# Kernel tuning notes

Measured on AMD Instinct MI355X. Metric: run time of the kernel, lower is better.

## Reference

```python
import jax, jax.numpy as jnp
import numpy as np

D_MODEL, D_FF, H, DK, DV = 1024, 4096, 16, 64, 64
B, S = 16, 512
EPS = 1e-6

def layer_norm(x, g, b):
    mu = jnp.mean(x, axis=-1, keepdims=True)
    var = jnp.var(x, axis=-1, keepdims=True)
    return (x - mu) / jnp.sqrt(var + EPS) * g + b

def setup_inputs() -> dict:
    key = jax.random.key(0)
    ks = jax.random.split(key, 16)
    def lin(k, fan_in, fan_out):
        lim = 1.0 / np.sqrt(fan_in)
        kw, kb = jax.random.split(k)
        W = jax.random.uniform(kw, (fan_in, fan_out), jnp.float32, -lim, lim)
        b = jax.random.uniform(kb, (fan_out,), jnp.float32, -lim, lim)
        return W, b
    Wq, bq = lin(ks[0], D_MODEL, DK * H)
    Wk, bk = lin(ks[1], D_MODEL, DK * H)
    Wv, bv = lin(ks[2], D_MODEL, DV * H)
    Wo, bo = lin(ks[3], DV * H, D_MODEL)
    w1, b1 = lin(ks[4], D_MODEL, D_FF)   # conv1d k=1 == pointwise linear
    w2, b2 = lin(ks[5], D_FF, D_MODEL)
    return {
        "enc_inputs": jax.random.normal(ks[6], (B, S, D_MODEL), jnp.float32),
        "Wq": Wq, "bq": bq, "Wk": Wk, "bk": bk, "Wv": Wv, "bv": bv,
        "Wo": Wo, "bo": bo,
        "ln1_g": jnp.ones((D_MODEL,), jnp.float32), "ln1_b": jnp.zeros((D_MODEL,), jnp.float32),
        "w1": w1, "b1": b1, "w2": w2, "b2": b2,
        "ln2_g": jnp.ones((D_MODEL,), jnp.float32), "ln2_b": jnp.zeros((D_MODEL,), jnp.float32),
        "mask": jax.random.randint(ks[7], (B, S), 0, 2, jnp.int32),
        "max_neighbors": S,
    }

def reference(enc_inputs, Wq, bq, Wk, bk, Wv, bv, Wo, bo, ln1_g, ln1_b,
              w1, b1, w2, b2, ln2_g, ln2_b, mask, max_neighbors):
    x = enc_inputs  # [B, S, D]
    residual = x
    # projections -> [B, H, S, d]
    q = (x @ Wq + bq).reshape(B, S, H, DK).transpose(0, 2, 1, 3)
    k = (x @ Wk + bk).reshape(B, S, H, DK).transpose(0, 2, 1, 3)
    v = (x @ Wv + bv).reshape(B, S, H, DV).transpose(0, 2, 1, 3)
    scores = jnp.einsum('bhqd,bhkd->bhqk', q, k) / np.sqrt(DK)
    pad = (mask == 0)[:, None, None, :]  # [B,1,1,S] broadcasts over heads & query
    scores = jnp.where(pad, jnp.float32(-1e9), scores)
    attn = jax.nn.softmax(scores, axis=-1)
    ctx = jnp.einsum('bhqk,bhkd->bhqd', attn, v)
    ctx = ctx.transpose(0, 2, 1, 3).reshape(B, S, H * DV)
    ctx = ctx @ Wo + bo
    ctx = layer_norm(ctx + residual, ln1_g, ln1_b)
    # position-wise FFN (conv1d kernel=1 == linear)
    ff = jax.nn.relu(ctx @ w1 + b1) @ w2 + b2
    out = layer_norm(ff + ctx, ln2_g, ln2_b)
    return out, attn
```

## Files before the change

kernel.cpp:

```cpp
#include <hip/hip_runtime.h>
#include <hip/hip_bf16.h>

typedef unsigned short u16;
typedef __bf16 bf16x8 __attribute__((ext_vector_type(8)));
typedef float f32x4 __attribute__((ext_vector_type(4)));

static __device__ __forceinline__ float b2f(u16 x) {
    unsigned int u = ((unsigned int)x) << 16;
    float f; __builtin_memcpy(&f, &u, 4); return f;
}
static __device__ __forceinline__ float b2f_u32(unsigned int u) {
    float f; __builtin_memcpy(&f, &u, 4); return f;
}
static __device__ __forceinline__ u16 f2b(float f) {
    unsigned int u; __builtin_memcpy(&u, &f, 4);
    unsigned int lsb = (u >> 16) & 1u;
    u += 0x7fffu + lsb;
    return (u16)(u >> 16);
}

static __device__ __forceinline__ void gload16(const u16* g, u16* l) {
    __builtin_amdgcn_global_load_lds(
        (const __attribute__((address_space(1))) unsigned int*)g,
        (__attribute__((address_space(3))) unsigned int*)l, 16, 0, 0);
}

__global__ __launch_bounds__(256) void transpose_f2b(const float* __restrict__ src,
                                                     u16* __restrict__ dst,
                                                     int R, int C) {
    __shared__ u16 tile[32][33];
    int c0 = blockIdx.x * 32, r0 = blockIdx.y * 32;
    int tx = threadIdx.x & 31, ty = threadIdx.x >> 5;
    for (int i = ty; i < 32; i += 8) {
        int r = r0 + i, c = c0 + tx;
        tile[i][tx] = (r < R && c < C) ? f2b(src[(long)r * C + c]) : (u16)0;
    }
    __syncthreads();
    for (int i = ty; i < 32; i += 8) {
        int c = c0 + i, r = r0 + tx;
        if (c < C && r < R) dst[(long)c * R + r] = tile[tx][i];
    }
}

__global__ __launch_bounds__(256) void concat3(const float* a, const float* b, const float* c,
                                               float* out) {
    int i = blockIdx.x * 256 + threadIdx.x;
    if (i < 1024) out[i] = a[i];
    else if (i < 2048) out[i] = b[i - 1024];
    else if (i < 3072) out[i] = c[i - 2048];
}

__global__ __launch_bounds__(256) void conv_f2b(const float* __restrict__ src,
                                                u16* __restrict__ dst, long n) {
    long i = ((long)blockIdx.x * 256 + threadIdx.x) * 4;
    if (i >= n) return;
    float4 f = *(const float4*)(src + i);
    ushort4 o;
    o.x = f2b(f.x); o.y = f2b(f.y); o.z = f2b(f.z); o.w = f2b(f.w);
    *(ushort4*)(dst + i) = o;
}

__global__ __launch_bounds__(512, 1) void gemm_bt256(
    const u16* __restrict__ A, const u16* __restrict__ B,
    const float* __restrict__ bias, u16* __restrict__ C,
    int M, int N, int K, int lda, int ldb, int ldc, int relu, int nbx) {
    __shared__ __align__(16) u16 lds[2][4][8192];

    int nwg = gridDim.x;
    int id = blockIdx.x;
    int swz = (id & 7) * (nwg >> 3) + (id >> 3);
    int bx = swz % nbx, by = swz / nbx;
    long m0 = (long)by * 256, n0 = (long)bx * 256;

    int tid = threadIdx.x, lane = tid & 63, wave = tid >> 6;
    int lrow = lane & 15, quad = lane >> 4;
    int wm2 = wave >> 2;
    int wn2 = wave & 3;

    int laneRd = (lrow * 64 + quad * 16) ^ (((lrow >> 3) & 1) << 5);
    int Sl = (lane * 16) ^ (((lane >> 5) & 1) << 5);
    int wr = (Sl >> 6) & 15;
    int wb = Sl & 63;

    f32x4 acc[8][4];
#pragma unroll
    for (int i = 0; i < 8; i++)
#pragma unroll
        for (int j = 0; j < 4; j++) acc[i][j] = (f32x4){0.f, 0.f, 0.f, 0.f};
    bf16x8 af[4][2], bfr[2][2];

#define STAGE_HT(nb, ht, kt) do {                                              \
    const char* _gb = ((ht) < 2)                                               \
        ? (const char*)(A + (m0 + (ht) * 128) * lda)                           \
        : (const char*)(B + (n0 + ((ht) - 2) * 128) * ldb);                    \
    long _ld = (long)(((ht) < 2) ? lda : ldb) * 2;                             \
    _Pragma("unroll")                                                          \
    for (int j = 0; j < 2; j++) {                                              \
        int sub = j * 8 + wave;                                                \
        int srow = (sub >> 1) * 16 + wr;                                       \
        int scolb = (sub & 1) * 64 + wb;                                       \
        gload16((const u16*)(_gb + (long)srow * _ld + (long)(kt) * 128 + scolb),\
                &lds[nb][ht][sub << 9]);                                       \
    }                                                                          \
} while (0)

#define DSLOAD_A(qm) do {                                                      \
    const char* _p = _ab + ((qm) << 14);                                       \
    _Pragma("unroll") for (int mi = 0; mi < 4; mi++)                           \
    _Pragma("unroll") for (int kk = 0; kk < 2; kk++)                           \
        af[mi][kk] = *(const bf16x8*)(_p + ((mi * 4 + kk) << 10));             \
} while (0)

#define DSLOAD_B(qn) do {                                                      \
    const char* _p = _bb + ((qn) << 14);                                       \
    _Pragma("unroll") for (int ni = 0; ni < 2; ni++)                           \
    _Pragma("unroll") for (int kk = 0; kk < 2; kk++)                           \
        bfr[ni][kk] = *(const bf16x8*)(_p + ((ni * 8 + kk) << 10));            \
} while (0)

#define DOMFMA(qm, qn) do {                                                    \
    __builtin_amdgcn_s_setprio(1);                                             \
    _Pragma("unroll") for (int mi = 0; mi < 4; mi++)                           \
    _Pragma("unroll") for (int ni = 0; ni < 2; ni++)                           \
    _Pragma("unroll") for (int kk = 0; kk < 2; kk++)                           \
        acc[(qm) * 4 + mi][(qn) * 2 + ni] =                                    \
            __builtin_amdgcn_mfma_f32_16x16x32_bf16(                           \
                af[mi][kk], bfr[ni][kk], acc[(qm) * 4 + mi][(qn) * 2 + ni],    \
                0, 0, 0);                                                      \
    __builtin_amdgcn_s_setprio(0);                                             \
} while (0)

#define MIDBAR()  do { __builtin_amdgcn_s_barrier(); __builtin_amdgcn_sched_barrier(0); } while (0)
#define ENDBAR()  do { __builtin_amdgcn_sched_barrier(0); __builtin_amdgcn_s_barrier(); } while (0)

    int NT = K >> 6;
    STAGE_HT(0, 0, 0);
    STAGE_HT(0, 2, 0);
    STAGE_HT(0, 1, 0);
    STAGE_HT(0, 3, 0);

    for (int t = 0; t < NT - 1; t++) {
        int cur = t & 1, nxt = cur ^ 1;
        const char* _ab = (const char*)&lds[cur][0][0] + (wm2 << 11) + laneRd;
        const char* _bb = (const char*)&lds[cur][2][0] + (wn2 << 11) + laneRd;
        STAGE_HT(nxt, 0, t + 1);
        asm volatile("s_waitcnt vmcnt(6)" ::: "memory");
        MIDBAR();
        DSLOAD_A(0); DSLOAD_B(0); DOMFMA(0, 0);
        ENDBAR();
        STAGE_HT(nxt, 2, t + 1);
        asm volatile("s_waitcnt vmcnt(6)" ::: "memory");
        MIDBAR();
        DSLOAD_A(1); DOMFMA(1, 0);
        ENDBAR();
        STAGE_HT(nxt, 1, t + 1);
        asm volatile("s_waitcnt vmcnt(6)" ::: "memory");
        MIDBAR();
        DSLOAD_B(1); DOMFMA(1, 1);
        ENDBAR();
        STAGE_HT(nxt, 3, t + 1);
        MIDBAR();
        DSLOAD_A(0); DOMFMA(0, 1);
        ENDBAR();
    }
    {
        int cur = (NT - 1) & 1;
        const char* _ab = (const char*)&lds[cur][0][0] + (wm2 << 11) + laneRd;
        const char* _bb = (const char*)&lds[cur][2][0] + (wn2 << 11) + laneRd;
        asm volatile("s_waitcnt vmcnt(4)" ::: "memory");
        MIDBAR();
        DSLOAD_A(0); DSLOAD_B(0); DOMFMA(0, 0);
        ENDBAR();
        asm volatile("s_waitcnt vmcnt(2)" ::: "memory");
        MIDBAR();
        DSLOAD_A(1); DOMFMA(1, 0);
        ENDBAR();
        asm volatile("s_waitcnt vmcnt(0)" ::: "memory");
        MIDBAR();
        DSLOAD_B(1); DOMFMA(1, 1);
        ENDBAR();
        DSLOAD_A(0); DOMFMA(0, 1);
    }

#pragma unroll
    for (int mg = 0; mg < 8; mg++) {
        long row0 = m0 + (long)(((mg >> 2) * 8 + (mg & 3) * 2 + wm2) * 16 + quad * 4);
#pragma unroll
        for (int ng = 0; ng < 4; ng++) {
            long col = n0 + ((ng >> 1) * 8 + (ng & 1) * 4 + wn2) * 16 + lrow;
            float bv = bias ? bias[col] : 0.f;
#pragma unroll
            for (int r = 0; r < 4; r++) {
                float v = acc[mg][ng][r] + bv;
                if (relu) v = fmaxf(v, 0.f);
                C[(row0 + r) * ldc + col] = f2b(v);
            }
        }
    }
#undef STAGE_HT
#undef DSLOAD_A
#undef DSLOAD_B
#undef DOMFMA
}

__global__ __launch_bounds__(512, 1) void gemm_btn(
    const u16* __restrict__ A, const u16* __restrict__ B,
    const float* __restrict__ bias, u16* __restrict__ C,
    int K, int lda, int ldb, int ldc, int relu, int nbx) {
    __shared__ __align__(16) u16 lds[2][3][8192];

    int nwg = gridDim.x;
    int id = blockIdx.x;
    int swz = (id & 7) * (nwg >> 3) + (id >> 3);
    int bx = swz % nbx, by = swz / nbx;
    long m0 = (long)by * 128, n0 = (long)bx * 256;

    int tid = threadIdx.x, lane = tid & 63, wave = tid >> 6;
    int lrow = lane & 15, quad = lane >> 4;
    int wm2 = wave >> 2;
    int wn2 = wave & 3;

    int laneRd = (lrow * 64 + quad * 16) ^ (((lrow >> 3) & 1) << 5);
    int Sl = (lane * 16) ^ (((lane >> 5) & 1) << 5);
    int wr = (Sl >> 6) & 15;
    int wb = Sl & 63;

    f32x4 acc[4][4];
#pragma unroll
    for (int i = 0; i < 4; i++)
#pragma unroll
        for (int j = 0; j < 4; j++) acc[i][j] = (f32x4){0.f, 0.f, 0.f, 0.f};
    bf16x8 af[4][2], bfr[2][2];

#define STAGE_HT(nb, ht, kt) do {                                              \
    const char* _gb = ((ht) == 0)                                              \
        ? (const char*)(A + m0 * lda)                                          \
        : (const char*)(B + (n0 + ((ht) - 1) * 128) * ldb);                    \
    long _ld = (long)(((ht) == 0) ? lda : ldb) * 2;                            \
    _Pragma("unroll")                                                          \
    for (int j = 0; j < 2; j++) {                                              \
        int sub = j * 8 + wave;                                                \
        int srow = (sub >> 1) * 16 + wr;                                       \
        int scolb = (sub & 1) * 64 + wb;                                       \
        gload16((const u16*)(_gb + (long)srow * _ld + (long)(kt) * 128 + scolb),\
                &lds[nb][ht][sub << 9]);                                       \
    }                                                                          \
} while (0)

#define DSLOAD_A() do {                                                        \
    _Pragma("unroll") for (int mi = 0; mi < 4; mi++)                           \
    _Pragma("unroll") for (int kk = 0; kk < 2; kk++)                           \
        af[mi][kk] = *(const bf16x8*)(_ab + ((mi * 4 + kk) << 10));            \
} while (0)

#define DSLOAD_B(qn) do {                                                      \
    const char* _p = _b0 + (qn) * 16384;                                       \
    _Pragma("unroll") for (int ni = 0; ni < 2; ni++)                           \
    _Pragma("unroll") for (int kk = 0; kk < 2; kk++)                           \
        bfr[ni][kk] = *(const bf16x8*)(_p + ((ni * 8 + kk) << 10));            \
} while (0)

#define DOMFMA(qn) do {                                                        \
    __builtin_amdgcn_s_setprio(1);                                             \
    _Pragma("unroll") for (int mi = 0; mi < 4; mi++)                           \
    _Pragma("unroll") for (int ni = 0; ni < 2; ni++)                           \
    _Pragma("unroll") for (int kk = 0; kk < 2; kk++)                           \
        acc[mi][(qn) * 2 + ni] =                                               \
            __builtin_amdgcn_mfma_f32_16x16x32_bf16(                           \
                af[mi][kk], bfr[ni][kk], acc[mi][(qn) * 2 + ni], 0, 0, 0);     \
    __builtin_amdgcn_s_setprio(0);                                             \
} while (0)

    int NT = K >> 6;
    STAGE_HT(0, 0, 0);
    STAGE_HT(0, 1, 0);
    STAGE_HT(0, 2, 0);

    for (int t = 0; t < NT - 1; t++) {
        int cur = t & 1, nxt = cur ^ 1;
        const char* _ab = (const char*)&lds[cur][0][0] + (wm2 << 11) + laneRd;
        const char* _b0 = (const char*)&lds[cur][1][0] + (wn2 << 11) + laneRd;
        STAGE_HT(nxt, 0, t + 1);
        asm volatile("s_waitcnt vmcnt(4)" ::: "memory");
        MIDBAR();
        DSLOAD_A(); DSLOAD_B(0); DOMFMA(0);
        ENDBAR();
        STAGE_HT(nxt, 1, t + 1);
        STAGE_HT(nxt, 2, t + 1);
        asm volatile("s_waitcnt vmcnt(6)" ::: "memory");
        MIDBAR();
        DSLOAD_B(1); DOMFMA(1);
        ENDBAR();
    }
    {
        int cur = (NT - 1) & 1;
        const char* _ab = (const char*)&lds[cur][0][0] + (wm2 << 11) + laneRd;
        const char* _b0 = (const char*)&lds[cur][1][0] + (wn2 << 11) + laneRd;
        asm volatile("s_waitcnt vmcnt(2)" ::: "memory");
        MIDBAR();
        DSLOAD_A(); DSLOAD_B(0); DOMFMA(0);
        ENDBAR();
        asm volatile("s_waitcnt vmcnt(0)" ::: "memory");
        MIDBAR();
        DSLOAD_B(1); DOMFMA(1);
    }

#pragma unroll
    for (int mi = 0; mi < 4; mi++) {
        long row0 = m0 + (long)((mi * 2 + wm2) * 16 + quad * 4);
#pragma unroll
        for (int ng = 0; ng < 4; ng++) {
            long col = n0 + ((ng >> 1) * 8 + (ng & 1) * 4 + wn2) * 16 + lrow;
            float bv = bias ? bias[col] : 0.f;
#pragma unroll
            for (int r = 0; r < 4; r++) {
                float v = acc[mi][ng][r] + bv;
                if (relu) v = fmaxf(v, 0.f);
                C[(row0 + r) * ldc + col] = f2b(v);
            }
        }
    }
#undef STAGE_HT
#undef DSLOAD_A
#undef DSLOAD_B
#undef DOMFMA
#undef MIDBAR
#undef ENDBAR
}

__global__ __launch_bounds__(256) void split_v(const u16* __restrict__ qkv,
                                               u16* __restrict__ vT) {
    __shared__ u16 tile[32][33];
    int bh = blockIdx.z;
    int b = bh >> 4, h = bh & 15;
    int s0 = blockIdx.x * 32;
    int d0 = blockIdx.y * 32;
    int tx = threadIdx.x & 31, ty = threadIdx.x >> 5;
    for (int i = ty; i < 32; i += 8)
        tile[i][tx] = qkv[((long)(b * 512 + s0 + i)) * 3072 + 2048 + h * 64 + d0 + tx];
    __syncthreads();
    for (int i = ty; i < 32; i += 8)
        vT[((long)bh * 64 + d0 + i) * 512 + s0 + tx] = tile[tx][i];
}

__global__ __launch_bounds__(256) void attn_fused(
    const u16* __restrict__ qkv, const u16* __restrict__ vT,
    const int* __restrict__ mask, float* __restrict__ attnOut,
    u16* __restrict__ ctx) {
    __shared__ __align__(16) u16 s_tile[64][72];
    __shared__ __align__(16) u16 s_p[4][16][136];
    __shared__ unsigned long long m_bits[8];

    int id = blockIdx.x;
    int t_ = id >> 3;
    int mtile = t_ & 7;
    int bh = (id & 7) + ((t_ >> 3) << 3);
    int b = bh >> 4, h = bh & 15;
    int tid = threadIdx.x, lane = tid & 63, wave = tid >> 6;
    int lrow = lane & 15, quad = lane >> 4;
    int m0 = mtile * 64;

    const u16* Qbase = qkv + (long)(b * 512) * 3072 + h * 64;
    const u16* Kbase = Qbase + 1024;

    {
        int i0 = wave * 64 + lane;
        unsigned long long bl0 = __ballot(mask[b * 512 + i0] != 0);
        if (lane == 0) m_bits[wave] = bl0;
        unsigned long long bl1 = __ballot(mask[b * 512 + 256 + i0] != 0);
        if (lane == 0) m_bits[4 + wave] = bl1;
    }

#pragma unroll
    for (int i = 0; i < 2; i++) {
        int idx = i * 256 + tid;
        int r = idx >> 3, c = (idx & 7) * 8;
        *(uint4*)&s_tile[r][c] = *(const uint4*)(Qbase + (long)(m0 + r) * 3072 + c);
    }
    __syncthreads();
    bf16x8 qf[2];
    qf[0] = *(const bf16x8*)&s_tile[wave * 16 + lrow][0 + quad * 8];
    qf[1] = *(const bf16x8*)&s_tile[wave * 16 + lrow][32 + quad * 8];

    f32x4 sacc[32];
#pragma unroll
    for (int t = 0; t < 32; t++) sacc[t] = (f32x4){0.f, 0.f, 0.f, 0.f};

#pragma unroll
    for (int t = 0; t < 32; t++) {
        const u16* krow = Kbase + (long)(t * 16 + lrow) * 3072 + quad * 8;
        bf16x8 b0 = *(const bf16x8*)krow;
        bf16x8 b1 = *(const bf16x8*)(krow + 32);
        sacc[t] = __builtin_amdgcn_mfma_f32_16x16x32_bf16(qf[0], b0, sacc[t], 0, 0, 0);
        sacc[t] = __builtin_amdgcn_mfma_f32_16x16x32_bf16(qf[1], b1, sacc[t], 0, 0, 0);
    }

    float mx[4] = {-3.0e38f, -3.0e38f, -3.0e38f, -3.0e38f};
#pragma unroll
    for (int t = 0; t < 32; t++) {
        int col = t * 16 + lrow;
        int on = (int)((m_bits[col >> 6] >> (col & 63)) & 1ull);
#pragma unroll
        for (int r = 0; r < 4; r++) {
            float s = on ? sacc[t][r] * 0.125f : -1e9f;
            sacc[t][r] = s;
            mx[r] = fmaxf(mx[r], s);
        }
    }
#pragma unroll
    for (int off = 1; off < 16; off <<= 1)
#pragma unroll
        for (int r = 0; r < 4; r++) mx[r] = fmaxf(mx[r], __shfl_xor(mx[r], off));
    float sm[4] = {0.f, 0.f, 0.f, 0.f};
#pragma unroll
    for (int t = 0; t < 32; t++)
#pragma unroll
        for (int r = 0; r < 4; r++) {
            float e = __expf(sacc[t][r] - mx[r]);
            sacc[t][r] = e;
            sm[r] += e;
        }
#pragma unroll
    for (int off = 1; off < 16; off <<= 1)
#pragma unroll
        for (int r = 0; r < 4; r++) sm[r] += __shfl_xor(sm[r], off);
#pragma unroll
    for (int r = 0; r < 4; r++) sm[r] = 1.0f / sm[r];
#pragma unroll
    for (int t = 0; t < 32; t++)
#pragma unroll
        for (int r = 0; r < 4; r++) sacc[t][r] *= sm[r];

    f32x4 cacc[4];
#pragma unroll
    for (int ni = 0; ni < 4; ni++) cacc[ni] = (f32x4){0.f, 0.f, 0.f, 0.f};
    const u16* vh = vT + (long)bh * 64 * 512;
    int prr = lane >> 5;
    int pcc = lane & 31;

    for (int nc = 0; nc < 4; nc++) {
#pragma unroll
        for (int t2 = 0; t2 < 8; t2++) {
            int t = nc * 8 + t2;
#pragma unroll
            for (int r = 0; r < 4; r++)
                s_p[wave][quad * 4 + r][t2 * 16 + lrow] = f2b(sacc[t][r]);
        }

        {
            float* abase = attnOut + (long)bh * 512 * 512
                         + (long)(m0 + wave * 16) * 512 + nc * 128;
#pragma unroll
            for (int i = 0; i < 8; i++) {
                int row = i * 2 + prr;
                uint2 pv = *(const uint2*)&s_p[wave][row][pcc * 4];
                float4 o;
                o.x = b2f_u32(pv.x << 16);
                o.y = b2f_u32(pv.x & 0xffff0000u);
                o.z = b2f_u32(pv.y << 16);
                o.w = b2f_u32(pv.y & 0xffff0000u);
                *(float4*)(abase + (long)row * 512 + pcc * 4) = o;
            }
        }

#pragma unroll
        for (int kk = 0; kk < 4; kk++) {
            bf16x8 pf = *(const bf16x8*)&s_p[wave][lrow][kk * 32 + quad * 8];
#pragma unroll
            for (int ni = 0; ni < 4; ni++) {
                bf16x8 vf = *(const bf16x8*)(vh + (long)(ni * 16 + lrow) * 512 + nc * 128 + kk * 32 + quad * 8);
                cacc[ni] = __builtin_amdgcn_mfma_f32_16x16x32_bf16(pf, vf, cacc[ni], 0, 0, 0);
            }
        }
    }

    u16* crow = ctx + (long)(b * 512 + m0 + wave * 16 + quad * 4) * 1024 + h * 64 + lrow;
#pragma unroll
    for (int ni = 0; ni < 4; ni++)
#pragma unroll
        for (int r = 0; r < 4; r++) crow[(long)r * 1024 + ni * 16] = f2b(cacc[ni][r]);
}

__global__ __launch_bounds__(256) void add_ln(const u16* __restrict__ a,
                                              const void* __restrict__ r, int r_fp32,
                                              const float* __restrict__ g,
                                              const float* __restrict__ beta,
                                              void* __restrict__ out, int out_fp32) {
    long row = blockIdx.x;
    const u16* pa = a + row * 1024;
    int tid = threadIdx.x;
    float v[4];
    float sum = 0.f, sq = 0.f;
#pragma unroll
    for (int j = 0; j < 4; j++) {
        int c = tid + j * 256;
        float rv = r_fp32 ? ((const float*)r)[row * 1024 + c]
                          : b2f(((const u16*)r)[row * 1024 + c]);
        float x = b2f(pa[c]) + rv;
        v[j] = x;
        sum += x;
        sq += x * x;
    }
#pragma unroll
    for (int off = 32; off >= 1; off >>= 1) {
        sum += __shfl_xor(sum, off);
        sq += __shfl_xor(sq, off);
    }
    __shared__ float red[2][4];
    int wave = tid >> 6, lane = tid & 63;
    if (lane == 0) { red[0][wave] = sum; red[1][wave] = sq; }
    __syncthreads();
    sum = red[0][0] + red[0][1] + red[0][2] + red[0][3];
    sq = red[1][0] + red[1][1] + red[1][2] + red[1][3];
    float mu = sum * (1.f / 1024.f);
    float var = sq * (1.f / 1024.f) - mu * mu;
    float rstd = rsqrtf(var + 1e-6f);
#pragma unroll
    for (int j = 0; j < 4; j++) {
        int c = tid + j * 256;
        float y = (v[j] - mu) * rstd * g[c] + beta[c];
        if (out_fp32) ((float*)out)[row * 1024 + c] = y;
        else ((u16*)out)[row * 1024 + c] = f2b(y);
    }
}

extern "C" void kernel_launch(void* const* d_in, const int* in_sizes, int n_in,
                              void* d_out, int out_size, void* d_ws, size_t ws_size,
                              hipStream_t stream) {
    const float* x   = (const float*)d_in[0];
    const float* Wq  = (const float*)d_in[1];
    const float* bq  = (const float*)d_in[2];
    const float* Wk  = (const float*)d_in[3];
    const float* bk  = (const float*)d_in[4];
    const float* Wv  = (const float*)d_in[5];
    const float* bv  = (const float*)d_in[6];
    const float* Wo  = (const float*)d_in[7];
    const float* bo  = (const float*)d_in[8];
    const float* g1  = (const float*)d_in[9];
    const float* be1 = (const float*)d_in[10];
    const float* w1  = (const float*)d_in[11];
    const float* b1  = (const float*)d_in[12];
    const float* w2  = (const float*)d_in[13];
    const float* b2  = (const float*)d_in[14];
    const float* g2  = (const float*)d_in[15];
    const float* be2 = (const float*)d_in[16];
    const int* mask  = (const int*)d_in[17];

    float* out = (float*)d_out;
    float* attn = out + (long)8192 * 1024;

    char* w = (char*)d_ws;
    auto alloc = [&](size_t bytes) {
        char* p = w;
        w += (bytes + 255) & ~(size_t)255;
        return p;
    };
    u16* WqkvT = (u16*)alloc(3072L * 1024 * 2);
    u16* WoT   = (u16*)alloc(1024L * 1024 * 2);
    u16* w1T   = (u16*)alloc(4096L * 1024 * 2);
    u16* w2T   = (u16*)alloc(1024L * 4096 * 2);
    float* bqkv = (float*)alloc(3072L * 4);
    u16* xb    = (u16*)alloc(8192L * 1024 * 2);
    char* P1 = alloc(8192L * 4096 * 2);
    u16* qkv = (u16*)P1;
    u16* ff  = (u16*)P1;
    char* P2 = alloc(256L * 64 * 512 * 2);
    u16* vT = (u16*)P2;
    u16* y2 = (u16*)P2;
    u16* ctx = (u16*)alloc(8192L * 1024 * 2);
    u16* x1  = (u16*)alloc(8192L * 1024 * 2);
    u16* y   = (u16*)alloc(8192L * 1024 * 2);

    dim3 blk(256);

    transpose_f2b<<<dim3(32, 32), blk, 0, stream>>>(Wq, WqkvT, 1024, 1024);
    transpose_f2b<<<dim3(32, 32), blk, 0, stream>>>(Wk, WqkvT + 1024L * 1024, 1024, 1024);
    transpose_f2b<<<dim3(32, 32), blk, 0, stream>>>(Wv, WqkvT + 2048L * 1024, 1024, 1024);
    transpose_f2b<<<dim3(32, 32), blk, 0, stream>>>(Wo, WoT, 1024, 1024);
    transpose_f2b<<<dim3(128, 32), blk, 0, stream>>>(w1, w1T, 1024, 4096);
    transpose_f2b<<<dim3(32, 128), blk, 0, stream>>>(w2, w2T, 4096, 1024);
    concat3<<<12, blk, 0, stream>>>(bq, bk, bv, bqkv);
    conv_f2b<<<8192, blk, 0, stream>>>(x, xb, 8192L * 1024);

    gemm_bt256<<<dim3(384), dim3(512), 0, stream>>>(
        xb, WqkvT, bqkv, qkv, 8192, 3072, 1024, 1024, 1024, 3072, 0, 12);

    split_v<<<dim3(16, 2, 256), blk, 0, stream>>>(qkv, vT);

    attn_fused<<<dim3(2048), blk, 0, stream>>>(qkv, vT, mask, attn, ctx);

    gemm_btn<<<dim3(256), dim3(512), 0, stream>>>(
        ctx, WoT, bo, y, 1024, 1024, 1024, 1024, 0, 4);

    add_ln<<<8192, blk, 0, stream>>>(y, x, 1, g1, be1, x1, 0);

    gemm_bt256<<<dim3(512), dim3(512), 0, stream>>>(
        x1, w1T, b1, ff, 8192, 4096, 1024, 1024, 1024, 4096, 1, 16);

    gemm_btn<<<dim3(256), dim3(512), 0, stream>>>(
        ff, w2T, b2, y2, 4096, 4096, 4096, 1024, 0, 4);

    add_ln<<<8192, blk, 0, stream>>>(y2, x1, 0, g2, be2, out, 1);
}
```

Baseline: 870.0 us.

## Stage K tiles through LDS with register prefetch in attention QK^T

Before this, each wave loaded the K rows it needed straight from global memory, so every one of the 4 waves fetched the whole K block. Now the block loads K cooperatively in 128-row chunks into a larger LDS tile, and the next chunk is prefetched into registers while the MFMAs run on the current one. The goal is to cut redundant global K traffic and hide load latency. In exchange it doubles the s_tile LDS footprint, adds barriers per chunk and holds extra prefetch registers, which could lower occupancy in a kernel that already keeps 32 accumulators live.

After: 829.2 us. 4.7% less time.

```diff
diff --git a/kernel.cpp b/kernel.cpp
--- a/kernel.cpp
+++ b/kernel.cpp
@@ -347,7 +347,7 @@
     const u16* __restrict__ qkv, const u16* __restrict__ vT,
     const int* __restrict__ mask, float* __restrict__ attnOut,
     u16* __restrict__ ctx) {
-    __shared__ __align__(16) u16 s_tile[64][72];
+    __shared__ __align__(16) u16 s_tile[128][72];
     __shared__ __align__(16) u16 s_p[4][16][136];
     __shared__ unsigned long long m_bits[8];
 
@@ -377,22 +377,48 @@
         int r = idx >> 3, c = (idx & 7) * 8;
         *(uint4*)&s_tile[r][c] = *(const uint4*)(Qbase + (long)(m0 + r) * 3072 + c);
     }
+    uint4 kreg[4];
+#pragma unroll
+    for (int i = 0; i < 4; i++) {
+        int idx = i * 256 + tid;
+        int r = idx >> 3, c = (idx & 7) * 8;
+        kreg[i] = *(const uint4*)(Kbase + (long)r * 3072 + c);
+    }
     __syncthreads();
     bf16x8 qf[2];
     qf[0] = *(const bf16x8*)&s_tile[wave * 16 + lrow][0 + quad * 8];
     qf[1] = *(const bf16x8*)&s_tile[wave * 16 + lrow][32 + quad * 8];
+    __syncthreads();
 
     f32x4 sacc[32];
 #pragma unroll
     for (int t = 0; t < 32; t++) sacc[t] = (f32x4){0.f, 0.f, 0.f, 0.f};
 
-#pragma unroll
-    for (int t = 0; t < 32; t++) {
-        const u16* krow = Kbase + (long)(t * 16 + lrow) * 3072 + quad * 8;
-        bf16x8 b0 = *(const bf16x8*)krow;
-        bf16x8 b1 = *(const bf16x8*)(krow + 32);
-        sacc[t] = __builtin_amdgcn_mfma_f32_16x16x32_bf16(qf[0], b0, sacc[t], 0, 0, 0);
-        sacc[t] = __builtin_amdgcn_mfma_f32_16x16x32_bf16(qf[1], b1, sacc[t], 0, 0, 0);
+    for (int nc = 0; nc < 4; nc++) {
+#pragma unroll
+        for (int i = 0; i < 4; i++) {
+            int idx = i * 256 + tid;
+            int r = idx >> 3, c = (idx & 7) * 8;
+            *(uint4*)&s_tile[r][c] = kreg[i];
+        }
+        __syncthreads();
+        if (nc < 3) {
+#pragma unroll
+            for (int i = 0; i < 4; i++) {
+                int idx = i * 256 + tid;
+                int r = idx >> 3, c = (idx & 7) * 8;
+                kreg[i] = *(const uint4*)(Kbase + (long)((nc + 1) * 128 + r) * 3072 + c);
+            }
+        }
+#pragma unroll
+        for (int ni = 0; ni < 8; ni++) {
+            bf16x8 b0 = *(const bf16x8*)&s_tile[ni * 16 + lrow][0 + quad * 8];
+            bf16x8 b1 = *(const bf16x8*)&s_tile[ni * 16 + lrow][32 + quad * 8];
+            int t = nc * 8 + ni;
+            sacc[t] = __builtin_amdgcn_mfma_f32_16x16x32_bf16(qf[0], b0, sacc[t], 0, 0, 0);
+            sacc[t] = __builtin_amdgcn_mfma_f32_16x16x32_bf16(qf[1], b1, sacc[t], 0, 0, 0);
+        }
+        __syncthreads();
     }
 
     float mx[4] = {-3.0e38f, -3.0e38f, -3.0e38f, -3.0e38f};
```

## Stage K and V tiles through double-buffered LDS in fused attention

Applied to the files above, without the earlier changes.

In the fused attention kernel, the four waves of a block no longer each read K and V straight from global memory. They now cooperatively load 64-row K and V tiles into a double-buffered shared-memory array, prefetching the next tile into registers while the current one feeds the MFMAs. P/V processing moves to 64-column chunks, with a smaller per-wave P buffer. The goal is to remove redundant global and L2 traffic for K and V, at the cost of one extra barrier per chunk and more shared-memory traffic.

Measured after the change: 812.8 us. -6.6%, faster.

```diff
diff --git a/kernel.cpp b/kernel.cpp
--- a/kernel.cpp
+++ b/kernel.cpp
@@ -347,8 +347,8 @@
     const u16* __restrict__ qkv, const u16* __restrict__ vT,
     const int* __restrict__ mask, float* __restrict__ attnOut,
     u16* __restrict__ ctx) {
-    __shared__ __align__(16) u16 s_tile[64][72];
-    __shared__ __align__(16) u16 s_p[4][16][136];
+    __shared__ __align__(16) u16 s_k[2][64][72];
+    __shared__ __align__(16) u16 s_p[4][16][68];
     __shared__ unsigned long long m_bits[8];
 
     int id = blockIdx.x;
@@ -362,6 +362,7 @@
 
     const u16* Qbase = qkv + (long)(b * 512) * 3072 + h * 64;
     const u16* Kbase = Qbase + 1024;
+    const u16* vh = vT + (long)bh * 64 * 512;
 
     {
         int i0 = wave * 64 + lane;
@@ -371,29 +372,45 @@
         if (lane == 0) m_bits[4 + wave] = bl1;
     }
 
-#pragma unroll
-    for (int i = 0; i < 2; i++) {
-        int idx = i * 256 + tid;
-        int r = idx >> 3, c = (idx & 7) * 8;
-        *(uint4*)&s_tile[r][c] = *(const uint4*)(Qbase + (long)(m0 + r) * 3072 + c);
-    }
+    int sr = tid >> 3, sc = (tid & 7) * 8;
+    int sr2 = (256 + tid) >> 3, sc2 = sc;
+    *(uint4*)&s_k[0][sr][sc]  = *(const uint4*)(Qbase + (long)(m0 + sr) * 3072 + sc);
+    *(uint4*)&s_k[0][sr2][sc2] = *(const uint4*)(Qbase + (long)(m0 + sr2) * 3072 + sc2);
+    uint4 kreg[2];
+    kreg[0] = *(const uint4*)(Kbase + (long)sr * 3072 + sc);
+    kreg[1] = *(const uint4*)(Kbase + (long)sr2 * 3072 + sc2);
     __syncthreads();
     bf16x8 qf[2];
-    qf[0] = *(const bf16x8*)&s_tile[wave * 16 + lrow][0 + quad * 8];
-    qf[1] = *(const bf16x8*)&s_tile[wave * 16 + lrow][32 + quad * 8];
+    qf[0] = *(const bf16x8*)&s_k[0][wave * 16 + lrow][0 + quad * 8];
+    qf[1] = *(const bf16x8*)&s_k[0][wave * 16 + lrow][32 + quad * 8];
+    __syncthreads();
 
     f32x4 sacc[32];
 #pragma unroll
     for (int t = 0; t < 32; t++) sacc[t] = (f32x4){0.f, 0.f, 0.f, 0.f};
 
-#pragma unroll
-    for (int t = 0; t < 32; t++) {
-        const u16* krow = Kbase + (long)(t * 16 + lrow) * 3072 + quad * 8;
-        bf16x8 b0 = *(const bf16x8*)krow;
-        bf16x8 b1 = *(const bf16x8*)(krow + 32);
-        sacc[t] = __builtin_amdgcn_mfma_f32_16x16x32_bf16(qf[0], b0, sacc[t], 0, 0, 0);
-        sacc[t] = __builtin_amdgcn_mfma_f32_16x16x32_bf16(qf[1], b1, sacc[t], 0, 0, 0);
-    }
+    for (int nc = 0; nc < 8; nc++) {
+        int buf = nc & 1;
+        *(uint4*)&s_k[buf][sr][sc]  = kreg[0];
+        *(uint4*)&s_k[buf][sr2][sc2] = kreg[1];
+        if (nc < 7) {
+            kreg[0] = *(const uint4*)(Kbase + (long)((nc + 1) * 64 + sr) * 3072 + sc);
+            kreg[1] = *(const uint4*)(Kbase + (long)((nc + 1) * 64 + sr2) * 3072 + sc2);
+        }
+        __syncthreads();
+#pragma unroll
+        for (int ni = 0; ni < 4; ni++) {
+            bf16x8 b0 = *(const bf16x8*)&s_k[buf][ni * 16 + lrow][0 + quad * 8];
+            bf16x8 b1 = *(const bf16x8*)&s_k[buf][ni * 16 + lrow][32 + quad * 8];
+            int t = nc * 4 + ni;
+            sacc[t] = __builtin_amdgcn_mfma_f32_16x16x32_bf16(qf[0], b0, sacc[t], 0, 0, 0);
+            sacc[t] = __builtin_amdgcn_mfma_f32_16x16x32_bf16(qf[1], b1, sacc[t], 0, 0, 0);
+        }
+    }
+
+    uint4 vreg[2];
+    vreg[0] = *(const uint4*)(vh + (long)sr * 512 + sc);
+    vreg[1] = *(const uint4*)(vh + (long)sr2 * 512 + sc2);
 
     float mx[4] = {-3.0e38f, -3.0e38f, -3.0e38f, -3.0e38f};
 #pragma unroll
@@ -434,41 +451,48 @@
     f32x4 cacc[4];
 #pragma unroll
     for (int ni = 0; ni < 4; ni++) cacc[ni] = (f32x4){0.f, 0.f, 0.f, 0.f};
-    const u16* vh = vT + (long)bh * 64 * 512;
-    int prr = lane >> 5;
-    int pcc = lane & 31;
-
-    for (int nc = 0; nc < 4; nc++) {
-#pragma unroll
-        for (int t2 = 0; t2 < 8; t2++) {
-            int t = nc * 8 + t2;
+    int prow = lane >> 4;
+    int pseg = lane & 15;
+
+    for (int nc = 0; nc < 8; nc++) {
+        int buf = nc & 1;
+        *(uint4*)&s_k[buf][sr][sc]  = vreg[0];
+        *(uint4*)&s_k[buf][sr2][sc2] = vreg[1];
+        if (nc < 7) {
+            vreg[0] = *(const uint4*)(vh + (long)sr * 512 + (nc + 1) * 64 + sc);
+            vreg[1] = *(const uint4*)(vh + (long)sr2 * 512 + (nc + 1) * 64 + sc2);
+        }
+#pragma unroll
+        for (int t2 = 0; t2 < 4; t2++) {
+            int t = nc * 4 + t2;
 #pragma unroll
             for (int r = 0; r < 4; r++)
                 s_p[wave][quad * 4 + r][t2 * 16 + lrow] = f2b(sacc[t][r]);
         }
+        __syncthreads();
 
         {
             float* abase = attnOut + (long)bh * 512 * 512
-                         + (long)(m0 + wave * 16) * 512 + nc * 128;
-#pragma unroll
-            for (int i = 0; i < 8; i++) {
-                int row = i * 2 + prr;
-                uint2 pv = *(const uint2*)&s_p[wave][row][pcc * 4];
+                         + (long)(m0 + wave * 16) * 512 + nc * 64;
+#pragma unroll
+            for (int i = 0; i < 4; i++) {
+                int row = i * 4 + prow;
+                uint2 pv = *(const uint2*)&s_p[wave][row][pseg * 4];
                 float4 o;
                 o.x = b2f_u32(pv.x << 16);
                 o.y = b2f_u32(pv.x & 0xffff0000u);
                 o.z = b2f_u32(pv.y << 16);
                 o.w = b2f_u32(pv.y & 0xffff0000u);
-                *(float4*)(abase + (long)row * 512 + pcc * 4) = o;
+                *(float4*)(abase + (long)row * 512 + pseg * 4) = o;
             }
         }
 
 #pragma unroll
-        for (int kk = 0; kk < 4; kk++) {
+        for (int kk = 0; kk < 2; kk++) {
             bf16x8 pf = *(const bf16x8*)&s_p[wave][lrow][kk * 32 + quad * 8];
 #pragma unroll
             for (int ni = 0; ni < 4; ni++) {
-                bf16x8 vf = *(const bf16x8*)(vh + (long)(ni * 16 + lrow) * 512 + nc * 128 + kk * 32 + quad * 8);
+                bf16x8 vf = *(const bf16x8*)&s_k[buf][ni * 16 + lrow][kk * 32 + quad * 8];
                 cacc[ni] = __builtin_amdgcn_mfma_f32_16x16x32_bf16(pf, vf, cacc[ni], 0, 0, 0);
             }
         }
```
